# Optimization experiments

Hardware: AMD Instinct MI355X
Metric: run time of the kernel (lower is better)

The kernel has to match this reference:

```python
import jax, jax.numpy as jnp
import numpy as np

DIM = 768
HEADS = 12
B, N = 1, 4096


def setup_inputs() -> dict:
    key = jax.random.key(0)
    k1, k2, k3 = jax.random.split(key, 3)
    x = jax.random.normal(k1, (B, N, DIM), dtype=jnp.float32)
    W_qkv = jax.random.normal(k2, (DIM, 3 * DIM), dtype=jnp.float32) * (DIM ** -0.5)
    W_out = jax.random.normal(k3, (DIM, DIM), dtype=jnp.float32) * (DIM ** -0.5)
    b_out = jnp.zeros((DIM,), dtype=jnp.float32)
    return {"x": x, "W_qkv": W_qkv, "W_out": W_out, "b_out": b_out}


def reference(x, W_qkv, W_out, b_out):
    b, n, dim = x.shape
    h = HEADS
    d = dim // h
    qkv = x @ W_qkv  # [b, n, 3*dim]
    q, k, v = jnp.split(qkv, 3, axis=-1)
    # 'b n (h d) -> b h n d'
    def to_heads(a):
        return a.reshape(b, n, h, d).transpose(0, 2, 1, 3)
    q, k, v = to_heads(q), to_heads(k), to_heads(v)
    # NOTE: original module computes self.scale but never applies it -> unscaled dots
    dots = jnp.einsum('bhid,bhjd->bhij', q, k)
    attn = jax.nn.softmax(dots, axis=-1)
    out = jnp.einsum('bhij,bhjd->bhid', attn, v)
    out = out.transpose(0, 2, 1, 3).reshape(b, n, dim)  # 'b h n d -> b n (h d)'
    return out @ W_out + b_out
```

## Files before the change

### kernel.cpp

```cpp
#include <hip/hip_runtime.h>

typedef unsigned short ushort_t;
typedef unsigned int uint_t;
typedef __bf16 bf16x8 __attribute__((ext_vector_type(8)));
typedef __bf16 bf16x4 __attribute__((ext_vector_type(4)));
typedef float f32x4 __attribute__((ext_vector_type(4)));
typedef ushort_t u16x4 __attribute__((ext_vector_type(4)));

#define NSEQ 4096
#define DIMM 768
#define NQKV 2304
#define HEADS 12
#define LOG2E 1.4426950408889634f

#if __has_builtin(__builtin_amdgcn_exp2f)
#define EXP2(x) __builtin_amdgcn_exp2f(x)
#else
#define EXP2(x) exp2f(x)
#endif


__device__ __forceinline__ ushort_t f2bf(float f) {
    uint_t u = __float_as_uint(f);
    u = u + 0x7fffu + ((u >> 16) & 1u);
    return (ushort_t)(u >> 16);
}
__device__ __forceinline__ f32x4 zero4() {
    f32x4 v = {0.f, 0.f, 0.f, 0.f};
    return v;
}

__global__ __launch_bounds__(256) void cvt_x_pack_kernel(const float* __restrict__ src,
                                                         ushort_t* __restrict__ dst) {
    int i = blockIdx.x * 256 + threadIdx.x;
    int row = i / (DIMM / 4);
    int k0 = (i - row * (DIMM / 4)) * 4;
    float4 v = *(const float4*)(&src[(size_t)row * DIMM + k0]);
    u16x4 p = { f2bf(v.x), f2bf(v.y), f2bf(v.z), f2bf(v.w) };
    size_t idx = ((size_t)(row >> 4) * (DIMM / 8) + (k0 >> 3)) * 128 + (row & 15) * 8 + (k0 & 7);
    *(u16x4*)(&dst[idx]) = p;
}

__global__ __launch_bounds__(256) void pack_w_kernel(
    const float* __restrict__ src, ushort_t* __restrict__ dst, int K, int N)
{
    __shared__ ushort_t Ls[64 * 72];
    const int t = threadIdx.x;
    const int bk = blockIdx.x * 64;
    const int bn = blockIdx.y * 64;
    const int tr = t >> 4, tc = t & 15;
#pragma unroll
    for (int i = 0; i < 4; ++i) {
        int r = tr + 16 * i;
        float4 v = *(const float4*)(&src[(size_t)(bk + r) * N + bn + tc * 4]);
        const float* vv = (const float*)&v;
#pragma unroll
        for (int j = 0; j < 4; ++j) Ls[(tc * 4 + j) * 72 + r] = f2bf(vv[j]);
    }
    __syncthreads();
    const int KB = K >> 3;
    const int n = t >> 2;
    const int ks = t & 3;
    const int gn = bn + n;
    size_t base = ((size_t)(gn >> 4) * KB + ((bk + ks * 16) >> 3)) * 128 + (gn & 15) * 8;
    *(uint4*)(&dst[base])       = *(const uint4*)(&Ls[n * 72 + ks * 16]);
    *(uint4*)(&dst[base + 128]) = *(const uint4*)(&Ls[n * 72 + ks * 16 + 8]);
}

__global__ __launch_bounds__(256) void qkv_gemm_kernel(
    const ushort_t* __restrict__ Ap, const ushort_t* __restrict__ Bp,
    ushort_t* __restrict__ Qp, ushort_t* __restrict__ Kp, ushort_t* __restrict__ Vp)
{
    const int t = threadIdx.x;
    const int lane = t & 63;
    const int w = t >> 6;
    const int m16 = lane & 15;
    const int g = lane >> 4;
    const int wrow = (w >> 1) * 64;
    const int wcol = (w & 1) * 64;
    const int bm = blockIdx.y * 128;
    const int bn = blockIdx.x * 128;
    const int amb = (bm + wrow) >> 4;
    const int bnb = (bn + wcol) >> 4;
    const int KB = DIMM / 8;
    const int which = bn / DIMM;

    f32x4 acc[4][4];
#pragma unroll
    for (int i = 0; i < 4; ++i)
#pragma unroll
        for (int j = 0; j < 4; ++j) acc[i][j] = zero4();

    if (which < 2) {
#pragma unroll 2
        for (int kt = 0; kt < 24; ++kt) {
            bf16x8 af[4], bfv[4];
#pragma unroll
            for (int mi = 0; mi < 4; ++mi)
                af[mi] = *(const bf16x8*)(&Ap[((size_t)(amb + mi) * KB + kt * 4 + g) * 128 + m16 * 8]);
#pragma unroll
            for (int nj = 0; nj < 4; ++nj)
                bfv[nj] = *(const bf16x8*)(&Bp[((size_t)(bnb + nj) * KB + kt * 4 + g) * 128 + m16 * 8]);
#pragma unroll
            for (int mi = 0; mi < 4; ++mi)
#pragma unroll
                for (int nj = 0; nj < 4; ++nj)
                    acc[mi][nj] = __builtin_amdgcn_mfma_f32_16x16x32_bf16(bfv[nj], af[mi], acc[mi][nj], 0, 0, 0);
        }
        ushort_t* dst = (which == 0) ? Qp : Kp;
        const float scale = (which == 0) ? LOG2E : 1.0f;
        const int cb = bn - which * DIMM + wcol;
        const int h = cb >> 6;
        const int ghi = g >> 1, glo = g & 1;
#pragma unroll
        for (int mi = 0; mi < 4; ++mi) {
            int sblk = amb + mi;
#pragma unroll
            for (int nj = 0; nj < 4; ++nj) {
                size_t idx = (((size_t)h * 256 + sblk) * 8 + nj * 2 + ghi) * 128 + m16 * 8 + glo * 4;
                u16x4 pk = { f2bf(acc[mi][nj][0] * scale), f2bf(acc[mi][nj][1] * scale),
                             f2bf(acc[mi][nj][2] * scale), f2bf(acc[mi][nj][3] * scale) };
                *(u16x4*)(&dst[idx]) = pk;
            }
        }
    } else {
#pragma unroll 2
        for (int kt = 0; kt < 24; ++kt) {
            bf16x8 af[4], bfv[4];
#pragma unroll
            for (int mi = 0; mi < 4; ++mi)
                af[mi] = *(const bf16x8*)(&Ap[((size_t)(amb + mi) * KB + kt * 4 + g) * 128 + m16 * 8]);
#pragma unroll
            for (int nj = 0; nj < 4; ++nj)
                bfv[nj] = *(const bf16x8*)(&Bp[((size_t)(bnb + nj) * KB + kt * 4 + g) * 128 + m16 * 8]);
#pragma unroll
            for (int mi = 0; mi < 4; ++mi)
#pragma unroll
                for (int nj = 0; nj < 4; ++nj)
                    acc[mi][nj] = __builtin_amdgcn_mfma_f32_16x16x32_bf16(af[mi], bfv[nj], acc[mi][nj], 0, 0, 0);
        }
        const int cb = bn - 2 * DIMM + wcol;
        const int h = cb >> 6;
        const int ghi = g >> 1, glo = g & 1;
        const int kb8 = (bm + wrow) >> 3;
#pragma unroll
        for (int mi = 0; mi < 4; ++mi) {
#pragma unroll
            for (int nj = 0; nj < 4; ++nj) {
                size_t idx = (((size_t)h * 512 + kb8 + mi * 2 + ghi) * 4 + nj) * 128 + m16 * 8 + glo * 4;
                u16x4 pk = { f2bf(acc[mi][nj][0]), f2bf(acc[mi][nj][1]),
                             f2bf(acc[mi][nj][2]), f2bf(acc[mi][nj][3]) };
                *(u16x4*)(&Vp[idx]) = pk;
            }
        }
    }
}

__global__ __launch_bounds__(256, 2) void attn_kernel(
    const ushort_t* __restrict__ Qp, const ushort_t* __restrict__ Kp,
    const ushort_t* __restrict__ Vp, float* __restrict__ Opart, float* __restrict__ Lpart,
    int niter)
{
    __shared__ ushort_t Ps[4][32 * 72];
    const int t = threadIdx.x;
    const int lane = t & 63;
    const int w = t >> 6;
    const int m16 = lane & 15;
    const int g = lane >> 4;
    const int h = blockIdx.y;
    const int half = blockIdx.z;
    const int qb = blockIdx.x * 128 + w * 32;
    const int qblk0 = qb >> 4;
    const int kblk0 = half * niter * 4;
    const int vblk0 = half * niter * 8;

    bf16x8 qf[2][2];
#pragma unroll
    for (int mi = 0; mi < 2; ++mi)
#pragma unroll
        for (int kd = 0; kd < 2; ++kd)
            qf[mi][kd] = *(const bf16x8*)(&Qp[(((size_t)h * 256 + qblk0 + mi) * 8 + kd * 4 + g) * 128 + m16 * 8]);

    const ushort_t* kpA = Kp + ((size_t)h * 256 + kblk0) * 1024 + g * 128 + m16 * 8;
    const ushort_t* kpB = kpA + 2048;
    const ushort_t* vpA = Vp + ((size_t)h * 512 + vblk0) * 512 + g * 512 + m16 * 8;
    const ushort_t* vpB = vpA + 2048;

    f32x4 oacc[2][4];
#pragma unroll
    for (int mi = 0; mi < 2; ++mi)
#pragma unroll
        for (int dj = 0; dj < 4; ++dj) oacc[mi][dj] = zero4();
    f32x4 lacc[2] = {zero4(), zero4()};

#pragma unroll 4
    for (int kt = 0; kt < niter; ++kt) {
        bf16x8 kf[4][2];
        kf[0][0] = *(const bf16x8*)(kpA);
        kf[0][1] = *(const bf16x8*)(kpA + 512);
        kf[1][0] = *(const bf16x8*)(kpA + 1024);
        kf[1][1] = *(const bf16x8*)(kpA + 1536);
        kf[2][0] = *(const bf16x8*)(kpB);
        kf[2][1] = *(const bf16x8*)(kpB + 512);
        kf[3][0] = *(const bf16x8*)(kpB + 1024);
        kf[3][1] = *(const bf16x8*)(kpB + 1536);
        bf16x8 vf[4][2];
#pragma unroll
        for (int dj = 0; dj < 4; ++dj) {
            vf[dj][0] = *(const bf16x8*)(vpA + dj * 128);
            vf[dj][1] = *(const bf16x8*)(vpB + dj * 128);
        }
        kpA += 4096; kpB += 4096; vpA += 4096; vpB += 4096;

#pragma unroll
        for (int nj = 0; nj < 4; ++nj) {
#pragma unroll
            for (int mi = 0; mi < 2; ++mi) {
                f32x4 st = zero4();
#pragma unroll
                for (int kd = 0; kd < 2; ++kd)
                    st = __builtin_amdgcn_mfma_f32_16x16x32_bf16(kf[nj][kd], qf[mi][kd], st, 0, 0, 0);
                f32x4 p;
#pragma unroll
                for (int r = 0; r < 4; ++r) p[r] = EXP2(st[r]);
                lacc[mi] += p;
                bf16x4 pk = { (__bf16)p[0], (__bf16)p[1], (__bf16)p[2], (__bf16)p[3] };
                *(bf16x4*)(&Ps[w][(mi * 16 + m16) * 72 + nj * 16 + g * 4]) = pk;
            }
        }
        bf16x8 pf[2][2];
#pragma unroll
        for (int mi = 0; mi < 2; ++mi)
#pragma unroll
            for (int kc = 0; kc < 2; ++kc)
                pf[mi][kc] = *(const bf16x8*)(&Ps[w][(mi * 16 + m16) * 72 + kc * 32 + g * 8]);
#pragma unroll
        for (int mi = 0; mi < 2; ++mi)
#pragma unroll
            for (int dj = 0; dj < 4; ++dj)
#pragma unroll
                for (int kc = 0; kc < 2; ++kc)
                    oacc[mi][dj] = __builtin_amdgcn_mfma_f32_16x16x32_bf16(pf[mi][kc], vf[dj][kc], oacc[mi][dj], 0, 0, 0);
    }

    float* Oph = Opart + (size_t)half * NSEQ * DIMM;
    float* Lph = Lpart + (size_t)half * HEADS * NSEQ + (size_t)h * NSEQ;
#pragma unroll
    for (int mi = 0; mi < 2; ++mi) {
        float l = (lacc[mi][0] + lacc[mi][1]) + (lacc[mi][2] + lacc[mi][3]);
        l += __shfl_xor(l, 16);
        l += __shfl_xor(l, 32);
        if (g == 0) Lph[qb + mi * 16 + m16] = l;
    }
#pragma unroll
    for (int mi = 0; mi < 2; ++mi) {
#pragma unroll
        for (int r = 0; r < 4; ++r) {
            int row = qb + mi * 16 + g * 4 + r;
#pragma unroll
            for (int dj = 0; dj < 4; ++dj)
                Oph[(size_t)row * DIMM + h * 64 + dj * 16 + m16] = oacc[mi][dj][r];
        }
    }
}

__global__ __launch_bounds__(256) void merge_kernel(
    const float* __restrict__ Opart, const float* __restrict__ Lpart,
    ushort_t* __restrict__ Xap, int nsplit)
{
    int i = blockIdx.x * 256 + threadIdx.x;
    int row = i / (DIMM / 4);
    int col0 = (i - row * (DIMM / 4)) * 4;
    int h = col0 >> 6;
    float l = 0.f;
    f32x4 o = zero4();
    for (int s = 0; s < nsplit; ++s) {
        l += Lpart[(size_t)s * HEADS * NSEQ + (size_t)h * NSEQ + row];
        f32x4 ov = *(const f32x4*)(&Opart[(size_t)s * NSEQ * DIMM + (size_t)row * DIMM + col0]);
        o += ov;
    }
    float inv = 1.0f / l;
    u16x4 p = { f2bf(o[0] * inv), f2bf(o[1] * inv), f2bf(o[2] * inv), f2bf(o[3] * inv) };
    size_t idx = ((size_t)(row >> 4) * (DIMM / 8) + (col0 >> 3)) * 128 + (row & 15) * 8 + (col0 & 7);
    *(u16x4*)(&Xap[idx]) = p;
}

__global__ __launch_bounds__(128) void out_gemm_kernel(
    const ushort_t* __restrict__ Ap, const ushort_t* __restrict__ Bp,
    const float* __restrict__ bias, float* __restrict__ out)
{
    const int t = threadIdx.x;
    const int lane = t & 63;
    const int w = t >> 6;
    const int m16 = lane & 15;
    const int g = lane >> 4;
    const int bm = blockIdx.y * 128;
    const int bn = blockIdx.x * 64;
    const int amb = (bm + w * 64) >> 4;
    const int bnb = bn >> 4;
    const int KB = DIMM / 8;

    f32x4 acc[4][4];
#pragma unroll
    for (int i = 0; i < 4; ++i)
#pragma unroll
        for (int j = 0; j < 4; ++j) acc[i][j] = zero4();

#pragma unroll 2
    for (int kt = 0; kt < 24; ++kt) {
        bf16x8 af[4], bfv[4];
#pragma unroll
        for (int mi = 0; mi < 4; ++mi)
            af[mi] = *(const bf16x8*)(&Ap[((size_t)(amb + mi) * KB + kt * 4 + g) * 128 + m16 * 8]);
#pragma unroll
        for (int nj = 0; nj < 4; ++nj)
            bfv[nj] = *(const bf16x8*)(&Bp[((size_t)(bnb + nj) * KB + kt * 4 + g) * 128 + m16 * 8]);
#pragma unroll
        for (int mi = 0; mi < 4; ++mi)
#pragma unroll
            for (int nj = 0; nj < 4; ++nj)
                acc[mi][nj] = __builtin_amdgcn_mfma_f32_16x16x32_bf16(af[mi], bfv[nj], acc[mi][nj], 0, 0, 0);
    }
#pragma unroll
    for (int mi = 0; mi < 4; ++mi) {
#pragma unroll
        for (int nj = 0; nj < 4; ++nj) {
            int col = bn + nj * 16 + m16;
            float bv = bias[col];
#pragma unroll
            for (int r = 0; r < 4; ++r) {
                int row = bm + w * 64 + mi * 16 + g * 4 + r;
                out[(size_t)row * DIMM + col] = acc[mi][nj][r] + bv;
            }
        }
    }
}

extern "C" void kernel_launch(void* const* d_in, const int* in_sizes, int n_in,
                              void* d_out, int out_size, void* d_ws, size_t ws_size,
                              hipStream_t stream) {
    (void)in_sizes; (void)n_in; (void)out_size;
    const float* X    = (const float*)d_in[0];
    const float* Wqkv = (const float*)d_in[1];
    const float* Wout = (const float*)d_in[2];
    const float* bout = (const float*)d_in[3];
    float* out = (float*)d_out;

    const size_t TSZ = (size_t)NSEQ * DIMM;
    const size_t fixed = TSZ * 2 * 5 + (size_t)NQKV * DIMM * 2 + (size_t)DIMM * DIMM * 2;
    const size_t per_split = TSZ * 4 + (size_t)HEADS * NSEQ * 4;
    const int nsplit = (ws_size >= fixed + 4 * per_split) ? 4 : 2;

    unsigned char* p = (unsigned char*)d_ws;
    ushort_t* Ap  = (ushort_t*)p; p += TSZ * 2;
    ushort_t* Wqp = (ushort_t*)p; p += (size_t)NQKV * DIMM * 2;
    ushort_t* Wop = (ushort_t*)p; p += (size_t)DIMM * DIMM * 2;
    ushort_t* Qp  = (ushort_t*)p; p += TSZ * 2;
    ushort_t* Kp  = (ushort_t*)p; p += TSZ * 2;
    ushort_t* Vp  = (ushort_t*)p; p += TSZ * 2;
    ushort_t* Xap = (ushort_t*)p; p += TSZ * 2;
    float* Opart  = (float*)p;    p += (size_t)nsplit * TSZ * 4;
    float* Lpart  = (float*)p;

    const int niter = (NSEQ / 64) / nsplit;

    cvt_x_pack_kernel<<<TSZ / 4 / 256, 256, 0, stream>>>(X, Ap);
    pack_w_kernel<<<dim3(DIMM / 64, NQKV / 64), 256, 0, stream>>>(Wqkv, Wqp, DIMM, NQKV);
    pack_w_kernel<<<dim3(DIMM / 64, DIMM / 64), 256, 0, stream>>>(Wout, Wop, DIMM, DIMM);
    qkv_gemm_kernel<<<dim3(NQKV / 128, NSEQ / 128), 256, 0, stream>>>(Ap, Wqp, Qp, Kp, Vp);
    attn_kernel<<<dim3(NSEQ / 128, HEADS, nsplit), 256, 0, stream>>>(Qp, Kp, Vp, Opart, Lpart, niter);
    merge_kernel<<<TSZ / 4 / 256, 256, 0, stream>>>(Opart, Lpart, Xap, nsplit);
    out_gemm_kernel<<<dim3(DIMM / 64, NSEQ / 128), 128, 0, stream>>>(Xap, Wop, bout, out);
}
```

Measured before the change: 210.5 us.

## Double-buffer register loads in GEMM and attention loops; merge prep kernels

Replaces the simple load-then-compute loops in the QKV GEMM, attention and output GEMM kernels with explicit two-stage register double buffering, so the global loads for the next K/V or K-tile are issued before the MFMAs on the current one. It also fuses the x conversion and the two weight-packing kernels into one prep kernel dispatched by block index, removing two launches. The cost is higher register pressure from two live fragment sets, which may cut occupancy (attention keeps launch_bounds 256,2). The attention loop assumes niter is even.

```diff
diff --git a/kernel.cpp b/kernel.cpp
--- a/kernel.cpp
+++ b/kernel.cpp
@@ -30,24 +30,10 @@
     return v;
 }
 
-__global__ __launch_bounds__(256) void cvt_x_pack_kernel(const float* __restrict__ src,
-                                                         ushort_t* __restrict__ dst) {
-    int i = blockIdx.x * 256 + threadIdx.x;
-    int row = i / (DIMM / 4);
-    int k0 = (i - row * (DIMM / 4)) * 4;
-    float4 v = *(const float4*)(&src[(size_t)row * DIMM + k0]);
-    u16x4 p = { f2bf(v.x), f2bf(v.y), f2bf(v.z), f2bf(v.w) };
-    size_t idx = ((size_t)(row >> 4) * (DIMM / 8) + (k0 >> 3)) * 128 + (row & 15) * 8 + (k0 & 7);
-    *(u16x4*)(&dst[idx]) = p;
-}
-
-__global__ __launch_bounds__(256) void pack_w_kernel(
-    const float* __restrict__ src, ushort_t* __restrict__ dst, int K, int N)
-{
-    __shared__ ushort_t Ls[64 * 72];
-    const int t = threadIdx.x;
-    const int bk = blockIdx.x * 64;
-    const int bn = blockIdx.y * 64;
+__device__ __forceinline__ void pack_w_tile(const float* __restrict__ src,
+                                            ushort_t* __restrict__ dst,
+                                            int K, int N, int bk, int bn, int t,
+                                            ushort_t* Ls) {
     const int tr = t >> 4, tc = t & 15;
 #pragma unroll
     for (int i = 0; i < 4; ++i) {
@@ -66,6 +52,43 @@
     *(uint4*)(&dst[base])       = *(const uint4*)(&Ls[n * 72 + ks * 16]);
     *(uint4*)(&dst[base + 128]) = *(const uint4*)(&Ls[n * 72 + ks * 16 + 8]);
 }
+
+#define CVT_BLOCKS   3072
+#define PW1_BLOCKS   (12 * 36)
+#define PW2_BLOCKS   (12 * 12)
+
+__global__ __launch_bounds__(256) void prep_kernel(
+    const float* __restrict__ X, const float* __restrict__ Wqkv, const float* __restrict__ Wout,
+    ushort_t* __restrict__ Ap, ushort_t* __restrict__ Wqp, ushort_t* __restrict__ Wop)
+{
+    __shared__ ushort_t Ls[64 * 72];
+    const int b = blockIdx.x;
+    const int t = threadIdx.x;
+    if (b < CVT_BLOCKS) {
+        int i = b * 256 + t;
+        int row = i / (DIMM / 4);
+        int k0 = (i - row * (DIMM / 4)) * 4;
+        float4 v = *(const float4*)(&X[(size_t)row * DIMM + k0]);
+        u16x4 p = { f2bf(v.x), f2bf(v.y), f2bf(v.z), f2bf(v.w) };
+        size_t idx = ((size_t)(row >> 4) * (DIMM / 8) + (k0 >> 3)) * 128 + (row & 15) * 8 + (k0 & 7);
+        *(u16x4*)(&Ap[idx]) = p;
+    } else if (b < CVT_BLOCKS + PW1_BLOCKS) {
+        int j = b - CVT_BLOCKS;
+        pack_w_tile(Wqkv, Wqp, DIMM, NQKV, (j % 12) * 64, (j / 12) * 64, t, Ls);
+    } else {
+        int j = b - CVT_BLOCKS - PW1_BLOCKS;
+        pack_w_tile(Wout, Wop, DIMM, DIMM, (j % 12) * 64, (j / 12) * 64, t, Ls);
+    }
+}
+
+#define QKV_LOAD(af, bfv, kt) do {                                                            \
+    _Pragma("unroll")                                                                         \
+    for (int mi = 0; mi < 4; ++mi)                                                            \
+        af[mi] = *(const bf16x8*)(&Ap[((size_t)(amb + mi) * KB + (kt) * 4 + g) * 128 + m16 * 8]); \
+    _Pragma("unroll")                                                                         \
+    for (int nj = 0; nj < 4; ++nj)                                                            \
+        bfv[nj] = *(const bf16x8*)(&Bp[((size_t)(bnb + nj) * KB + (kt) * 4 + g) * 128 + m16 * 8]); \
+} while (0)
 
 __global__ __launch_bounds__(256) void qkv_gemm_kernel(
     const ushort_t* __restrict__ Ap, const ushort_t* __restrict__ Bp,
@@ -91,21 +114,23 @@
 #pragma unroll
         for (int j = 0; j < 4; ++j) acc[i][j] = zero4();
 
+    bf16x8 af0[4], bf0[4], af1[4], bf1[4];
+    QKV_LOAD(af0, bf0, 0);
+
     if (which < 2) {
-#pragma unroll 2
-        for (int kt = 0; kt < 24; ++kt) {
-            bf16x8 af[4], bfv[4];
+        for (int kt = 0; kt < 24; kt += 2) {
+            QKV_LOAD(af1, bf1, kt + 1);
 #pragma unroll
             for (int mi = 0; mi < 4; ++mi)
-                af[mi] = *(const bf16x8*)(&Ap[((size_t)(amb + mi) * KB + kt * 4 + g) * 128 + m16 * 8]);
-#pragma unroll
-            for (int nj = 0; nj < 4; ++nj)
-                bfv[nj] = *(const bf16x8*)(&Bp[((size_t)(bnb + nj) * KB + kt * 4 + g) * 128 + m16 * 8]);
+#pragma unroll
+                for (int nj = 0; nj < 4; ++nj)
+                    acc[mi][nj] = __builtin_amdgcn_mfma_f32_16x16x32_bf16(bf0[nj], af0[mi], acc[mi][nj], 0, 0, 0);
+            if (kt + 2 < 24) QKV_LOAD(af0, bf0, kt + 2);
 #pragma unroll
             for (int mi = 0; mi < 4; ++mi)
 #pragma unroll
                 for (int nj = 0; nj < 4; ++nj)
-                    acc[mi][nj] = __builtin_amdgcn_mfma_f32_16x16x32_bf16(bfv[nj], af[mi], acc[mi][nj], 0, 0, 0);
+                    acc[mi][nj] = __builtin_amdgcn_mfma_f32_16x16x32_bf16(bf1[nj], af1[mi], acc[mi][nj], 0, 0, 0);
         }
         ushort_t* dst = (which == 0) ? Qp : Kp;
         const float scale = (which == 0) ? LOG2E : 1.0f;
@@ -124,20 +149,19 @@
             }
         }
     } else {
-#pragma unroll 2
-        for (int kt = 0; kt < 24; ++kt) {
-            bf16x8 af[4], bfv[4];
+        for (int kt = 0; kt < 24; kt += 2) {
+            QKV_LOAD(af1, bf1, kt + 1);
 #pragma unroll
             for (int mi = 0; mi < 4; ++mi)
-                af[mi] = *(const bf16x8*)(&Ap[((size_t)(amb + mi) * KB + kt * 4 + g) * 128 + m16 * 8]);
-#pragma unroll
-            for (int nj = 0; nj < 4; ++nj)
-                bfv[nj] = *(const bf16x8*)(&Bp[((size_t)(bnb + nj) * KB + kt * 4 + g) * 128 + m16 * 8]);
+#pragma unroll
+                for (int nj = 0; nj < 4; ++nj)
+                    acc[mi][nj] = __builtin_amdgcn_mfma_f32_16x16x32_bf16(af0[mi], bf0[nj], acc[mi][nj], 0, 0, 0);
+            if (kt + 2 < 24) QKV_LOAD(af0, bf0, kt + 2);
 #pragma unroll
             for (int mi = 0; mi < 4; ++mi)
 #pragma unroll
                 for (int nj = 0; nj < 4; ++nj)
-                    acc[mi][nj] = __builtin_amdgcn_mfma_f32_16x16x32_bf16(af[mi], bfv[nj], acc[mi][nj], 0, 0, 0);
+                    acc[mi][nj] = __builtin_amdgcn_mfma_f32_16x16x32_bf16(af1[mi], bf1[nj], acc[mi][nj], 0, 0, 0);
         }
         const int cb = bn - 2 * DIMM + wcol;
         const int h = cb >> 6;
@@ -155,6 +179,54 @@
         }
     }
 }
+
+#define ATTN_LOAD(kf, vf, ka, kb, va, vb) do {           \
+    kf[0][0] = *(const bf16x8*)(ka);                     \
+    kf[0][1] = *(const bf16x8*)((ka) + 512);             \
+    kf[1][0] = *(const bf16x8*)((ka) + 1024);            \
+    kf[1][1] = *(const bf16x8*)((ka) + 1536);            \
+    kf[2][0] = *(const bf16x8*)(kb);                     \
+    kf[2][1] = *(const bf16x8*)((kb) + 512);             \
+    kf[3][0] = *(const bf16x8*)((kb) + 1024);            \
+    kf[3][1] = *(const bf16x8*)((kb) + 1536);            \
+    _Pragma("unroll")                                    \
+    for (int dj = 0; dj < 4; ++dj) {                     \
+        vf[dj][0] = *(const bf16x8*)((va) + dj * 128);   \
+        vf[dj][1] = *(const bf16x8*)((vb) + dj * 128);   \
+    }                                                    \
+} while (0)
+
+#define ATTN_COMPUTE(kf, vf) do {                                                              \
+    _Pragma("unroll")                                                                          \
+    for (int nj = 0; nj < 4; ++nj) {                                                           \
+        _Pragma("unroll")                                                                      \
+        for (int mi = 0; mi < 2; ++mi) {                                                       \
+            f32x4 st = zero4();                                                                \
+            _Pragma("unroll")                                                                  \
+            for (int kd = 0; kd < 2; ++kd)                                                     \
+                st = __builtin_amdgcn_mfma_f32_16x16x32_bf16(kf[nj][kd], qf[mi][kd], st, 0, 0, 0); \
+            f32x4 p;                                                                           \
+            _Pragma("unroll")                                                                  \
+            for (int r = 0; r < 4; ++r) p[r] = EXP2(st[r]);                                    \
+            lacc[mi] += p;                                                                     \
+            bf16x4 pk = { (__bf16)p[0], (__bf16)p[1], (__bf16)p[2], (__bf16)p[3] };            \
+            *(bf16x4*)(&Ps[w][(mi * 16 + m16) * 72 + nj * 16 + g * 4]) = pk;                   \
+        }                                                                                      \
+    }                                                                                          \
+    bf16x8 pf[2][2];                                                                           \
+    _Pragma("unroll")                                                                          \
+    for (int mi = 0; mi < 2; ++mi)                                                             \
+        _Pragma("unroll")                                                                      \
+        for (int kc = 0; kc < 2; ++kc)                                                         \
+            pf[mi][kc] = *(const bf16x8*)(&Ps[w][(mi * 16 + m16) * 72 + kc * 32 + g * 8]);     \
+    _Pragma("unroll")                                                                          \
+    for (int mi = 0; mi < 2; ++mi)                                                             \
+        _Pragma("unroll")                                                                      \
+        for (int dj = 0; dj < 4; ++dj)                                                         \
+            _Pragma("unroll")                                                                  \
+            for (int kc = 0; kc < 2; ++kc)                                                     \
+                oacc[mi][dj] = __builtin_amdgcn_mfma_f32_16x16x32_bf16(pf[mi][kc], vf[dj][kc], oacc[mi][dj], 0, 0, 0); \
+} while (0)
 
 __global__ __launch_bounds__(256, 2) void attn_kernel(
     const ushort_t* __restrict__ Qp, const ushort_t* __restrict__ Kp,
@@ -193,54 +265,19 @@
         for (int dj = 0; dj < 4; ++dj) oacc[mi][dj] = zero4();
     f32x4 lacc[2] = {zero4(), zero4()};
 
-#pragma unroll 4
-    for (int kt = 0; kt < niter; ++kt) {
-        bf16x8 kf[4][2];
-        kf[0][0] = *(const bf16x8*)(kpA);
-        kf[0][1] = *(const bf16x8*)(kpA + 512);
-        kf[1][0] = *(const bf16x8*)(kpA + 1024);
-        kf[1][1] = *(const bf16x8*)(kpA + 1536);
-        kf[2][0] = *(const bf16x8*)(kpB);
-        kf[2][1] = *(const bf16x8*)(kpB + 512);
-        kf[3][0] = *(const bf16x8*)(kpB + 1024);
-        kf[3][1] = *(const bf16x8*)(kpB + 1536);
-        bf16x8 vf[4][2];
-#pragma unroll
-        for (int dj = 0; dj < 4; ++dj) {
-            vf[dj][0] = *(const bf16x8*)(vpA + dj * 128);
-            vf[dj][1] = *(const bf16x8*)(vpB + dj * 128);
-        }
+    bf16x8 kf0[4][2], vf0[4][2], kf1[4][2], vf1[4][2];
+    ATTN_LOAD(kf0, vf0, kpA, kpB, vpA, vpB);
+    kpA += 4096; kpB += 4096; vpA += 4096; vpB += 4096;
+
+    for (int kt = 0; kt < niter; kt += 2) {
+        ATTN_LOAD(kf1, vf1, kpA, kpB, vpA, vpB);
         kpA += 4096; kpB += 4096; vpA += 4096; vpB += 4096;
-
-#pragma unroll
-        for (int nj = 0; nj < 4; ++nj) {
-#pragma unroll
-            for (int mi = 0; mi < 2; ++mi) {
-                f32x4 st = zero4();
-#pragma unroll
-                for (int kd = 0; kd < 2; ++kd)
-                    st = __builtin_amdgcn_mfma_f32_16x16x32_bf16(kf[nj][kd], qf[mi][kd], st, 0, 0, 0);
-                f32x4 p;
-#pragma unroll
-                for (int r = 0; r < 4; ++r) p[r] = EXP2(st[r]);
-                lacc[mi] += p;
-                bf16x4 pk = { (__bf16)p[0], (__bf16)p[1], (__bf16)p[2], (__bf16)p[3] };
-                *(bf16x4*)(&Ps[w][(mi * 16 + m16) * 72 + nj * 16 + g * 4]) = pk;
-            }
-        }
-        bf16x8 pf[2][2];
-#pragma unroll
-        for (int mi = 0; mi < 2; ++mi)
-#pragma unroll
-            for (int kc = 0; kc < 2; ++kc)
-                pf[mi][kc] = *(const bf16x8*)(&Ps[w][(mi * 16 + m16) * 72 + kc * 32 + g * 8]);
-#pragma unroll
-        for (int mi = 0; mi < 2; ++mi)
-#pragma unroll
-            for (int dj = 0; dj < 4; ++dj)
-#pragma unroll
-                for (int kc = 0; kc < 2; ++kc)
-                    oacc[mi][dj] = __builtin_amdgcn_mfma_f32_16x16x32_bf16(pf[mi][kc], vf[dj][kc], oacc[mi][dj], 0, 0, 0);
+        ATTN_COMPUTE(kf0, vf0);
+        if (kt + 2 < niter) {
+            ATTN_LOAD(kf0, vf0, kpA, kpB, vpA, vpB);
+            kpA += 4096; kpB += 4096; vpA += 4096; vpB += 4096;
+        }
+        ATTN_COMPUTE(kf1, vf1);
     }
 
     float* Oph = Opart + (size_t)half * NSEQ * DIMM;
@@ -285,6 +322,15 @@
     *(u16x4*)(&Xap[idx]) = p;
 }
 
+#define OUT_LOAD(af, bfv, kt) do {                                                            \
+    _Pragma("unroll")                                                                         \
+    for (int mi = 0; mi < 4; ++mi)                                                            \
+        af[mi] = *(const bf16x8*)(&Ap[((size_t)(amb + mi) * KB + (kt) * 4 + g) * 128 + m16 * 8]); \
+    _Pragma("unroll")                                                                         \
+    for (int nj = 0; nj < 4; ++nj)                                                            \
+        bfv[nj] = *(const bf16x8*)(&Bp[((size_t)(bnb + nj) * KB + (kt) * 4 + g) * 128 + m16 * 8]); \
+} while (0)
+
 __global__ __launch_bounds__(128) void out_gemm_kernel(
     const ushort_t* __restrict__ Ap, const ushort_t* __restrict__ Bp,
     const float* __restrict__ bias, float* __restrict__ out)
@@ -306,20 +352,21 @@
 #pragma unroll
         for (int j = 0; j < 4; ++j) acc[i][j] = zero4();
 
-#pragma unroll 2
-    for (int kt = 0; kt < 24; ++kt) {
-        bf16x8 af[4], bfv[4];
+    bf16x8 af0[4], bf0[4], af1[4], bf1[4];
+    OUT_LOAD(af0, bf0, 0);
+    for (int kt = 0; kt < 24; kt += 2) {
+        OUT_LOAD(af1, bf1, kt + 1);
 #pragma unroll
         for (int mi = 0; mi < 4; ++mi)
-            af[mi] = *(const bf16x8*)(&Ap[((size_t)(amb + mi) * KB + kt * 4 + g) * 128 + m16 * 8]);
-#pragma unroll
-        for (int nj = 0; nj < 4; ++nj)
-            bfv[nj] = *(const bf16x8*)(&Bp[((size_t)(bnb + nj) * KB + kt * 4 + g) * 128 + m16 * 8]);
+#pragma unroll
+            for (int nj = 0; nj < 4; ++nj)
+                acc[mi][nj] = __builtin_amdgcn_mfma_f32_16x16x32_bf16(af0[mi], bf0[nj], acc[mi][nj], 0, 0, 0);
+        if (kt + 2 < 24) OUT_LOAD(af0, bf0, kt + 2);
 #pragma unroll
         for (int mi = 0; mi < 4; ++mi)
 #pragma unroll
             for (int nj = 0; nj < 4; ++nj)
-                acc[mi][nj] = __builtin_amdgcn_mfma_f32_16x16x32_bf16(af[mi], bfv[nj], acc[mi][nj], 0, 0, 0);
+                acc[mi][nj] = __builtin_amdgcn_mfma_f32_16x16x32_bf16(af1[mi], bf1[nj], acc[mi][nj], 0, 0, 0);
     }
 #pragma unroll
     for (int mi = 0; mi < 4; ++mi) {
@@ -364,9 +411,7 @@
 
     const int niter = (NSEQ / 64) / nsplit;
 
-    cvt_x_pack_kernel<<<TSZ / 4 / 256, 256, 0, stream>>>(X, Ap);
-    pack_w_kernel<<<dim3(DIMM / 64, NQKV / 64), 256, 0, stream>>>(Wqkv, Wqp, DIMM, NQKV);
-    pack_w_kernel<<<dim3(DIMM / 64, DIMM / 64), 256, 0, stream>>>(Wout, Wop, DIMM, DIMM);
+    prep_kernel<<<CVT_BLOCKS + PW1_BLOCKS + PW2_BLOCKS, 256, 0, stream>>>(X, Wqkv, Wout, Ap, Wqp, Wop);
     qkv_gemm_kernel<<<dim3(NQKV / 128, NSEQ / 128), 256, 0, stream>>>(Ap, Wqp, Qp, Kp, Vp);
     attn_kernel<<<dim3(NSEQ / 128, HEADS, nsplit), 256, 0, stream>>>(Qp, Kp, Vp, Opart, Lpart, niter);
     merge_kernel<<<TSZ / 4 / 256, 256, 0, stream>>>(Opart, Lpart, Xap, nsplit);
```

New measurement: 205.9 us. -2.2%, faster.
